# Kernel optimization log

Measured on AMD Instinct MI355X. Metric: run time of the kernel, lower is better.

Reference implementation:

```python
import jax, jax.numpy as jnp
import numpy as np

HEAD_SIZE = 64

def setup_inputs() -> dict:
    key = jax.random.key(0)
    kx, kq, kk, kv = jax.random.split(key, 4)
    n_embd = 1024
    x = jax.random.normal(kx, (4, 2048, n_embd), dtype=jnp.float32)
    s = 1.0 / np.sqrt(n_embd)
    Wq = jax.random.normal(kq, (HEAD_SIZE, n_embd), dtype=jnp.float32) * s
    Wk = jax.random.normal(kk, (HEAD_SIZE, n_embd), dtype=jnp.float32) * s
    Wv = jax.random.normal(kv, (HEAD_SIZE, n_embd), dtype=jnp.float32) * s
    return {"x": x, "Wq": Wq, "Wk": Wk, "Wv": Wv}

def reference(x, Wq, Wk, Wv):
    # x: [B, T, C]; W*: [head_size, C] (torch nn.Linear weight layout, y = x @ W.T)
    B, T, C = x.shape
    q = jnp.einsum('btc,hc->bth', x, Wq)  # [B, T, H]
    k = jnp.einsum('btc,hc->bth', x, Wk)
    v = jnp.einsum('btc,hc->bth', x, Wv)
    att = jnp.einsum('bqh,bkh->bqk', q, k) / jnp.sqrt(jnp.float32(HEAD_SIZE))
    causal = jnp.tril(jnp.ones((T, T), dtype=bool))  # [T, T]
    att = jnp.where(causal, att, -jnp.inf)
    att = jax.nn.softmax(att, axis=-1)
    out = jnp.einsum('bqk,bkh->bqh', att, v)  # [B, T, H]
    return out
```

## Files before the change

### kernel.cpp

```cpp
#include <hip/hip_runtime.h>
#include <hip/hip_bf16.h>

#define NB 4
#define TT 2048
#define CC 1024
#define HS 64
#define L2E 1.4426950408889634f

typedef __attribute__((ext_vector_type(8))) short short8;
typedef __attribute__((ext_vector_type(4))) short short4v;
typedef __attribute__((ext_vector_type(4))) float floatx4;
typedef __attribute__((ext_vector_type(2))) float floatx2;

__device__ __forceinline__ short f2bf(float f) {
  union { float f; unsigned u; } x; x.f = f;
  unsigned r = (x.u + 0x7fffu + ((x.u >> 16) & 1u)) >> 16;
  return (short)r;
}

__device__ __forceinline__ short8 pack_bf16x8(floatx4 a, floatx4 b) {
  union { __hip_bfloat162 h[4]; short8 s; } u;
  u.h[0] = __float22bfloat162_rn(make_float2(a[0], a[1]));
  u.h[1] = __float22bfloat162_rn(make_float2(a[2], a[3]));
  u.h[2] = __float22bfloat162_rn(make_float2(b[0], b[1]));
  u.h[3] = __float22bfloat162_rn(make_float2(b[2], b[3]));
  return u.s;
}

#define KC 64
#define WTS 72

__global__ __launch_bounds__(768) void qkv_proj(const float* __restrict__ x,
                                                const float* __restrict__ wq,
                                                const float* __restrict__ wk,
                                                const float* __restrict__ wv,
                                                short* __restrict__ qb,
                                                short* __restrict__ kbuf,
                                                short* __restrict__ vtb) {
  __shared__ __align__(16) short wt[2][192 * WTS];
  __shared__ __align__(16) short xs[2][32 * WTS];

  const int tid  = threadIdx.x;
  const int lane = tid & 63;
  const int w    = tid >> 6;
  const int col  = lane & 15;
  const int quad = lane >> 4;
  const int row32 = blockIdx.x * 32;
  const int rg = w / 6;
  const int cg = w % 6;
  const int mat   = cg >> 1;
  const int hbase = (cg & 1) * 32;

  const int o0 = tid >> 3,         kk0 = (tid & 7) * 8;
  const int o1 = (768 + tid) >> 3, kk1 = ((768 + tid) & 7) * 8;
  const float* wsrc0 = (o0 < 64 ? wq + (size_t)o0 * CC
                                : wk + (size_t)(o0 - 64) * CC) + kk0;
  const float* wsrc1 = (o1 < 128 ? wk + (size_t)(o1 - 64) * CC
                                 : wv + (size_t)(o1 - 128) * CC) + kk1;
  const int xr = tid >> 3, xk = (tid & 7) * 8;
  const float* xsrc = x + (size_t)(row32 + xr) * CC + xk;

  floatx4 wa0 = *(const floatx4*)(wsrc0);
  floatx4 wc0 = *(const floatx4*)(wsrc0 + 4);
  floatx4 wa1 = *(const floatx4*)(wsrc1);
  floatx4 wc1 = *(const floatx4*)(wsrc1 + 4);
  floatx4 xA[2], xC[2];
  if (tid < 256) {
    xA[0] = *(const floatx4*)(xsrc);       xC[0] = *(const floatx4*)(xsrc + 4);
    xA[1] = *(const floatx4*)(xsrc + KC);  xC[1] = *(const floatx4*)(xsrc + KC + 4);
  }

  *(short8*)(&wt[0][o0 * WTS + kk0]) = pack_bf16x8(wa0, wc0);
  *(short8*)(&wt[0][o1 * WTS + kk1]) = pack_bf16x8(wa1, wc1);
  if (tid < 256) *(short8*)(&xs[0][xr * WTS + xk]) = pack_bf16x8(xA[0], xC[0]);
  __syncthreads();

  floatx4 acc0 = (floatx4){0.f, 0.f, 0.f, 0.f};
  floatx4 acc1 = (floatx4){0.f, 0.f, 0.f, 0.f};
  const int arow  = (rg * 16 + col) * WTS + quad * 8;
  const int brow0 = (cg * 32 + col) * WTS + quad * 8;
  const int brow1 = (cg * 32 + 16 + col) * WTS + quad * 8;

#pragma unroll 2
  for (int ch = 0; ch < 16; ++ch) {
    const int cur = ch & 1;
    if (ch < 15) {
      const int k0 = (ch + 1) * KC;
      wa0 = *(const floatx4*)(wsrc0 + k0);
      wc0 = *(const floatx4*)(wsrc0 + k0 + 4);
      wa1 = *(const floatx4*)(wsrc1 + k0);
      wc1 = *(const floatx4*)(wsrc1 + k0 + 4);
    }
    if (ch < 14 && tid < 256) {
      const int k0 = (ch + 2) * KC;
      xA[cur] = *(const floatx4*)(xsrc + k0);
      xC[cur] = *(const floatx4*)(xsrc + k0 + 4);
    }
#pragma unroll
    for (int kb2 = 0; kb2 < 2; ++kb2) {
      short8 a  = *(const short8*)(&xs[cur][arow + kb2 * 32]);
      short8 b0 = *(const short8*)(&wt[cur][brow0 + kb2 * 32]);
      short8 b1 = *(const short8*)(&wt[cur][brow1 + kb2 * 32]);
      acc0 = __builtin_amdgcn_mfma_f32_16x16x32_bf16(a, b0, acc0, 0, 0, 0);
      acc1 = __builtin_amdgcn_mfma_f32_16x16x32_bf16(a, b1, acc1, 0, 0, 0);
    }
    if (ch < 15) {
      __syncthreads();
      const int nxt = cur ^ 1;
      *(short8*)(&wt[nxt][o0 * WTS + kk0]) = pack_bf16x8(wa0, wc0);
      *(short8*)(&wt[nxt][o1 * WTS + kk1]) = pack_bf16x8(wa1, wc1);
      if (tid < 256)
        *(short8*)(&xs[nxt][xr * WTS + xk]) = pack_bf16x8(xA[nxt & 1], xC[nxt & 1]);
      __syncthreads();
    }
  }

  const int h0 = hbase + col;
  const int h1 = hbase + 16 + col;
  if (mat == 2) {
    int b = row32 >> 11;
    int t = (row32 & (TT - 1)) + rg * 16 + quad * 4;
    short4v o;
    o[0] = f2bf(acc0[0]); o[1] = f2bf(acc0[1]); o[2] = f2bf(acc0[2]); o[3] = f2bf(acc0[3]);
    *(short4v*)(vtb + (size_t)(b * HS + h0) * TT + t) = o;
    o[0] = f2bf(acc1[0]); o[1] = f2bf(acc1[1]); o[2] = f2bf(acc1[2]); o[3] = f2bf(acc1[3]);
    *(short4v*)(vtb + (size_t)(b * HS + h1) * TT + t) = o;
  } else {
    short* dst = (mat == 0) ? qb : kbuf;
    float s = (mat == 0) ? 0.125f : 1.0f;
#pragma unroll
    for (int r = 0; r < 4; ++r) {
      size_t row = (size_t)(row32 + rg * 16 + quad * 4 + r);
      dst[row * HS + h0] = f2bf(acc0[r] * s);
      dst[row * HS + h1] = f2bf(acc1[r] * s);
    }
  }
}

#define PST 72

__global__ __launch_bounds__(512) void attn(const short* __restrict__ qb,
                                            const short* __restrict__ kb,
                                            const short* __restrict__ vtb,
                                            float* __restrict__ out) {
  __shared__ __align__(16) short pt[8][2][16 * PST];
  __shared__ float cl[8][16];
  __shared__ __align__(16) float co[8][16][64];

  const int tid  = threadIdx.x;
  const int lane = tid & 63;
  const int w    = tid >> 6;
  const int col  = lane & 15;
  const int quad = lane >> 4;
  const int b  = blockIdx.x >> 7;
  const int qt = blockIdx.x & 127;
  const int t0 = qt * 16;

  const short* qbase = qb + (size_t)(b * TT + t0) * HS;
  const short* kbase = kb + (size_t)b * TT * HS;
  const short* vbase = vtb + (size_t)b * HS * TT;

  short8 qf0 = *(const short8*)(qbase + col * HS + quad * 8);
  short8 qf1 = *(const short8*)(qbase + col * HS + 32 + quad * 8);

  floatx4 oacc[4];
#pragma unroll
  for (int i = 0; i < 4; ++i) oacc[i] = (floatx4){0.f, 0.f, 0.f, 0.f};
  float lsum[4] = {0.f, 0.f, 0.f, 0.f};

  const int Nc = (t0 + 16 + 63) >> 6;

  short8 knA[4], knB[4];
  if (w < Nc) {
    const short* kp = kbase + (size_t)(w * 64) * HS + quad * 8;
#pragma unroll
    for (int j = 0; j < 4; ++j) {
      knA[j] = *(const short8*)(kp + (size_t)(j * 16 + col) * HS);
      knB[j] = *(const short8*)(kp + (size_t)(j * 16 + col) * HS + 32);
    }
  }

  int parity = 0;
  for (int c = w; c < Nc; c += 8, parity ^= 1) {
    const int kb0 = c * 64;

    floatx4 st[4];
#pragma unroll
    for (int j = 0; j < 4; ++j) st[j] = (floatx4){0.f, 0.f, 0.f, 0.f};
#pragma unroll
    for (int j = 0; j < 4; ++j) {
      st[j] = __builtin_amdgcn_mfma_f32_16x16x32_bf16(qf0, knA[j], st[j], 0, 0, 0);
      st[j] = __builtin_amdgcn_mfma_f32_16x16x32_bf16(qf1, knB[j], st[j], 0, 0, 0);
    }

    if (c + 8 < Nc) {
      const short* kpn = kbase + (size_t)((c + 8) * 64) * HS + quad * 8;
#pragma unroll
      for (int j = 0; j < 4; ++j) {
        knA[j] = *(const short8*)(kpn + (size_t)(j * 16 + col) * HS);
        knB[j] = *(const short8*)(kpn + (size_t)(j * 16 + col) * HS + 32);
      }
    }

    if (kb0 + 63 > t0) {
#pragma unroll
      for (int j = 0; j < 4; ++j) {
        int kcol = kb0 + j * 16 + col;
#pragma unroll
        for (int r = 0; r < 4; ++r)
          if (kcol > t0 + quad * 4 + r) st[j][r] = -1e30f;
      }
    }

    float pv[4][4];
#pragma unroll
    for (int j = 0; j < 4; ++j)
#pragma unroll
      for (int r = 0; r < 4; ++r)
        pv[j][r] = exp2f(st[j][r] * L2E);
#pragma unroll
    for (int r = 0; r < 4; ++r)
      lsum[r] += (pv[0][r] + pv[1][r]) + (pv[2][r] + pv[3][r]);

    short* pw = &pt[w][parity][0];
#pragma unroll
    for (int j = 0; j < 4; ++j)
#pragma unroll
      for (int r = 0; r < 4; ++r)
        pw[(quad * 4 + r) * PST + j * 16 + col] = f2bf(pv[j][r]);
    short8 af0 = *(const short8*)(pw + col * PST + quad * 8);
    short8 af1 = *(const short8*)(pw + col * PST + 32 + quad * 8);

#pragma unroll
    for (int ht = 0; ht < 4; ++ht) {
      const short* vp = vbase + (size_t)(ht * 16 + col) * TT + kb0 + quad * 8;
      short8 vf0 = *(const short8*)(vp);
      short8 vf1 = *(const short8*)(vp + 32);
      oacc[ht] = __builtin_amdgcn_mfma_f32_16x16x32_bf16(af0, vf0, oacc[ht], 0, 0, 0);
      oacc[ht] = __builtin_amdgcn_mfma_f32_16x16x32_bf16(af1, vf1, oacc[ht], 0, 0, 0);
    }
  }

#pragma unroll
  for (int r = 0; r < 4; ++r) {
#pragma unroll
    for (int off = 8; off; off >>= 1) lsum[r] += __shfl_xor(lsum[r], off);
    if (col == 0) cl[w][quad * 4 + r] = lsum[r];
#pragma unroll
    for (int ht = 0; ht < 4; ++ht)
      co[w][quad * 4 + r][ht * 16 + col] = oacc[ht][r];
  }
  __syncthreads();

  const int crow = tid >> 5;
  const int ch   = (tid & 31) << 1;
  float L = 0.f;
  floatx2 a = (floatx2){0.f, 0.f};
#pragma unroll
  for (int w2 = 0; w2 < 8; ++w2) {
    L += cl[w2][crow];
    floatx2 ov = *(const floatx2*)&co[w2][crow][ch];
    a[0] += ov[0]; a[1] += ov[1];
  }
  float inv = 1.0f / L;
  floatx2 res = (floatx2){a[0] * inv, a[1] * inv};
  *(floatx2*)(out + (size_t)(b * TT + t0 + crow) * HS + ch) = res;
}

extern "C" void kernel_launch(void* const* d_in, const int* in_sizes, int n_in,
                              void* d_out, int out_size, void* d_ws, size_t ws_size,
                              hipStream_t stream) {
  const float* x  = (const float*)d_in[0];
  const float* wq = (const float*)d_in[1];
  const float* wk = (const float*)d_in[2];
  const float* wv = (const float*)d_in[3];
  float* out = (float*)d_out;

  char* ws = (char*)d_ws;
  short* qbf = (short*)ws;
  short* kbf = (short*)(ws + 1048576);
  short* vtb = (short*)(ws + 2097152);

  hipLaunchKernelGGL(qkv_proj, dim3(256), dim3(768), 0, stream,
                     x, wq, wk, wv, qbf, kbf, vtb);
  hipLaunchKernelGGL(attn, dim3(512), dim3(512), 0, stream, qbf, kbf, vtb, out);
}
```

Before: 123.1 us.

## Reorder attention blocks longest-first, hoist V loads, fuse exp/pack, set occupancy hint

```diff
diff --git a/kernel.cpp b/kernel.cpp
--- a/kernel.cpp
+++ b/kernel.cpp
@@ -139,10 +139,10 @@
 
 #define PST 72
 
-__global__ __launch_bounds__(512) void attn(const short* __restrict__ qb,
-                                            const short* __restrict__ kb,
-                                            const short* __restrict__ vtb,
-                                            float* __restrict__ out) {
+__global__ __launch_bounds__(512, 4) void attn(const short* __restrict__ qb,
+                                               const short* __restrict__ kb,
+                                               const short* __restrict__ vtb,
+                                               float* __restrict__ out) {
   __shared__ __align__(16) short pt[8][2][16 * PST];
   __shared__ float cl[8][16];
   __shared__ __align__(16) float co[8][16][64];
@@ -152,8 +152,8 @@
   const int w    = tid >> 6;
   const int col  = lane & 15;
   const int quad = lane >> 4;
-  const int b  = blockIdx.x >> 7;
-  const int qt = blockIdx.x & 127;
+  const int b  = blockIdx.x & 3;
+  const int qt = 127 - (blockIdx.x >> 2);
   const int t0 = qt * 16;
 
   const short* qbase = qb + (size_t)(b * TT + t0) * HS;
@@ -191,6 +191,14 @@
     for (int j = 0; j < 4; ++j) {
       st[j] = __builtin_amdgcn_mfma_f32_16x16x32_bf16(qf0, knA[j], st[j], 0, 0, 0);
       st[j] = __builtin_amdgcn_mfma_f32_16x16x32_bf16(qf1, knB[j], st[j], 0, 0, 0);
+    }
+
+    short8 vfA[4], vfB[4];
+#pragma unroll
+    for (int ht = 0; ht < 4; ++ht) {
+      const short* vp = vbase + (size_t)(ht * 16 + col) * TT + kb0 + quad * 8;
+      vfA[ht] = *(const short8*)(vp);
+      vfB[ht] = *(const short8*)(vp + 32);
     }
 
     if (c + 8 < Nc) {
@@ -202,42 +210,37 @@
       }
     }
 
-    if (kb0 + 63 > t0) {
-#pragma unroll
-      for (int j = 0; j < 4; ++j) {
+    const bool diag = (kb0 + 63 > t0);
+    short* pw = &pt[w][parity][0];
+
+#pragma unroll
+    for (int j = 0; j < 4; ++j) {
+      if (diag) {
         int kcol = kb0 + j * 16 + col;
 #pragma unroll
         for (int r = 0; r < 4; ++r)
           if (kcol > t0 + quad * 4 + r) st[j][r] = -1e30f;
       }
-    }
-
-    float pv[4][4];
-#pragma unroll
-    for (int j = 0; j < 4; ++j)
-#pragma unroll
-      for (int r = 0; r < 4; ++r)
-        pv[j][r] = exp2f(st[j][r] * L2E);
-#pragma unroll
-    for (int r = 0; r < 4; ++r)
-      lsum[r] += (pv[0][r] + pv[1][r]) + (pv[2][r] + pv[3][r]);
-
-    short* pw = &pt[w][parity][0];
-#pragma unroll
-    for (int j = 0; j < 4; ++j)
-#pragma unroll
-      for (int r = 0; r < 4; ++r)
-        pw[(quad * 4 + r) * PST + j * 16 + col] = f2bf(pv[j][r]);
+      float p0 = exp2f(st[j][0] * L2E);
+      float p1 = exp2f(st[j][1] * L2E);
+      float p2 = exp2f(st[j][2] * L2E);
+      float p3 = exp2f(st[j][3] * L2E);
+      lsum[0] += p0; lsum[1] += p1; lsum[2] += p2; lsum[3] += p3;
+      union { __hip_bfloat162 h; short s[2]; } uA, uB;
+      uA.h = __float22bfloat162_rn(make_float2(p0, p1));
+      uB.h = __float22bfloat162_rn(make_float2(p2, p3));
+      pw[(quad * 4 + 0) * PST + j * 16 + col] = uA.s[0];
+      pw[(quad * 4 + 1) * PST + j * 16 + col] = uA.s[1];
+      pw[(quad * 4 + 2) * PST + j * 16 + col] = uB.s[0];
+      pw[(quad * 4 + 3) * PST + j * 16 + col] = uB.s[1];
+    }
     short8 af0 = *(const short8*)(pw + col * PST + quad * 8);
     short8 af1 = *(const short8*)(pw + col * PST + 32 + quad * 8);
 
 #pragma unroll
     for (int ht = 0; ht < 4; ++ht) {
-      const short* vp = vbase + (size_t)(ht * 16 + col) * TT + kb0 + quad * 8;
-      short8 vf0 = *(const short8*)(vp);
-      short8 vf1 = *(const short8*)(vp + 32);
-      oacc[ht] = __builtin_amdgcn_mfma_f32_16x16x32_bf16(af0, vf0, oacc[ht], 0, 0, 0);
-      oacc[ht] = __builtin_amdgcn_mfma_f32_16x16x32_bf16(af1, vf1, oacc[ht], 0, 0, 0);
+      oacc[ht] = __builtin_amdgcn_mfma_f32_16x16x32_bf16(af0, vfA[ht], oacc[ht], 0, 0, 0);
+      oacc[ht] = __builtin_amdgcn_mfma_f32_16x16x32_bf16(af1, vfB[ht], oacc[ht], 0, 0, 0);
     }
   }
 
```

New measurement: 119.5 us. -3.0%, faster.
